# Optimization experiments

Measured on AMD Instinct MI355X. Metric: run time of the kernel, lower is better.

## Reference

```python
import jax, jax.numpy as jnp
import numpy as np

V_NT, V_RULE, E, H = 200, 500, 1024, 1024  # H == E so cat([nt_emb, prod_emb]) == E + H
B, T, L_NL, L_ENV = 32, 128, 512, 512


def setup_inputs() -> dict:
    key = jax.random.key(0)
    ks = jax.random.split(key, 20)
    s = 0.02
    return {
        'init_prod': jax.random.randint(ks[0], (B,), 0, V_RULE),
        'nt_ids': jax.random.randint(ks[1], (T, B), 0, V_NT),
        'h0': jax.random.normal(ks[2], (B, H), jnp.float32),
        'c0': jax.random.normal(ks[3], (B, H), jnp.float32),
        'nl_encoding': jax.random.normal(ks[4], (B, L_NL, H), jnp.float32),
        'env_encoding': jax.random.normal(ks[5], (B, L_ENV, H), jnp.float32),
        'nt_emb': jax.random.normal(ks[6], (V_NT, E), jnp.float32) * s,
        'rule_emb': jax.random.normal(ks[7], (V_RULE, E), jnp.float32) * s,
        'W_ih': jax.random.normal(ks[8], (4 * H, E + H), jnp.float32) * s,
        'W_hh': jax.random.normal(ks[9], (4 * H, H), jnp.float32) * s,
        'b_ih': jnp.zeros((4 * H,), jnp.float32),
        'b_hh': jnp.zeros((4 * H,), jnp.float32),
        'Wz': jax.random.normal(ks[10], (H, 2 * H), jnp.float32) * s,
        'bz': jnp.zeros((H,), jnp.float32),
        'We': jax.random.normal(ks[11], (H, 2 * H), jnp.float32) * s,
        'be': jnp.zeros((H,), jnp.float32),
        'Wc': jax.random.normal(ks[12], (H, 3 * H), jnp.float32) * s,
        'bc': jnp.zeros((H,), jnp.float32),
    }


def _attention(query, context, W, b):
    # query: (B, H), context: (B, L, H)
    scores = jnp.einsum('bh,blh->bl', query, context)          # bmm(output, context^T)
    attn = jax.nn.softmax(scores, axis=-1)                     # softmax over input_len
    mix = jnp.einsum('bl,blh->bh', attn, context)              # bmm(attn, context)
    out = jnp.tanh(jnp.concatenate([mix, query], axis=-1) @ W.T + b)
    return out, attn


def reference(init_prod, nt_ids, h0, c0, nl_encoding, env_encoding,
              nt_emb, rule_emb, W_ih, W_hh, b_ih, b_hh,
              Wz, bz, We, be, Wc, bc):
    last_prod = rule_emb[init_prod]  # (B, E); never updated in the source loop

    def step(carry, nt_t):
        h, c = carry
        x = jnp.concatenate([nt_emb[nt_t], last_prod], axis=-1)  # (B, E+H)
        gates = x @ W_ih.T + b_ih + h @ W_hh.T + b_hh             # (B, 4H)
        i, f, g, o = jnp.split(gates, 4, axis=-1)                 # torch gate order i,f,g,o
        i = jax.nn.sigmoid(i); f = jax.nn.sigmoid(f)
        g = jnp.tanh(g); o = jax.nn.sigmoid(o)
        c_new = f * c + i * g
        h_new = o * jnp.tanh(c_new)
        st = h_new                                                # (B, H)
        zt, _ = _attention(st, nl_encoding, Wz, bz)               # nl cross-attention
        et, _ = _attention(zt, env_encoding, We, be)              # env cross-attention
        ct = jnp.tanh(jnp.concatenate([st, zt, et], axis=-1) @ Wc.T + bc)
        return (h_new, c_new), ct

    _, cts = jax.lax.scan(step, (h0, c0), nt_ids)  # cts: (T, B, H)
    return cts
```

## Files before the change

### kernel.cpp

```cpp
#include <hip/hip_runtime.h>
#include <hip/hip_bf16.h>

typedef _Float16 f16;
typedef __attribute__((ext_vector_type(8))) _Float16 f16x8;
typedef __attribute__((ext_vector_type(4))) float f32x4;
typedef __attribute__((ext_vector_type(4))) unsigned int u32x4;
typedef __attribute__((ext_vector_type(2))) int i32x2;

#define TT 128
#define LSTM_BLOCKS 128

__device__ __forceinline__ float sigmoidf_(float x) { return 1.0f / (1.0f + __expf(-x)); }

__global__ __launch_bounds__(256) void k_f2h(const float* __restrict__ in,
                                             f16* __restrict__ out, long n4) {
  long i = (long)blockIdx.x * 256 + threadIdx.x;
  if (i >= n4) return;
  float4 v = ((const float4*)in)[i];
  out[i*4+0] = (f16)v.x; out[i*4+1] = (f16)v.y;
  out[i*4+2] = (f16)v.z; out[i*4+3] = (f16)v.w;
}

__global__ __launch_bounds__(256) void k_gather_prod(const float* __restrict__ rule_emb,
                                                     const int* __restrict__ init_prod,
                                                     f16* __restrict__ out) {
  int i = blockIdx.x * 256 + threadIdx.x;
  int b = i >> 10, k = i & 1023;
  out[i] = (f16)rule_emb[(long)init_prod[b] * 1024 + k];
}

__global__ __launch_bounds__(256) void k_h0(const float* __restrict__ h0,
                                            f16* __restrict__ st) {
  int i = blockIdx.x * 256 + threadIdx.x;
  int b = i >> 10, k = i & 1023;
  st[(long)(k >> 3) * 256 + b * 8 + (k & 7)] = (f16)h0[i];
}

__global__ __launch_bounds__(256) void k_zero(int* p, int n) {
  for (int i = threadIdx.x; i < n; i += 256) p[i] = 0;
}

__global__ __launch_bounds__(256) void k_transpose(const float* __restrict__ in,
                                                   f16* __restrict__ outT,
                                                   f16* __restrict__ outN) {
  __shared__ float tile[32][33];
  const int b  = blockIdx.z;
  const int l0 = blockIdx.x * 32, h0 = blockIdx.y * 32;
  in   += (long)b * 512 * 1024;
  outT += (long)b * 1024 * 512;
  outN += (long)b * 512 * 1024;
  const int c = threadIdx.x & 31, r = threadIdx.x >> 5;
#pragma unroll
  for (int p = 0; p < 4; ++p) {
    float v = in[(long)(l0 + r + p*8) * 1024 + h0 + c];
    tile[r + p*8][c] = v;
    outN[(long)(l0 + r + p*8) * 1024 + h0 + c] = (f16)v;
  }
  __syncthreads();
#pragma unroll
  for (int p = 0; p < 4; ++p)
    outT[(long)(h0 + r + p*8) * 512 + l0 + c] = (f16)tile[c][r + p*8];
}

__global__ __launch_bounds__(256) void k_gemm(
    const f16* __restrict__ A, long lda, long sA,
    const f16* __restrict__ B, long ldb, long sB,
    float* __restrict__ outF, long ldF, long sF, long sSl,
    f16* __restrict__ outH, long ldH, long sH,
    f16* __restrict__ outH2, long ldH2, long sH2,
    f16* __restrict__ out2, long ld2, long s2,
    const float* __restrict__ bias1, const float* __restrict__ bias2,
    int M, int N, int K, int act, int bmod, int zdiv, int ilv)
{
  __shared__ __align__(16) f16 As[128][40];
  __shared__ __align__(16) f16 Bs[128][40];
  const int tid = threadIdx.x;
  const int w = tid >> 6, lane = tid & 63;
  const int wm = (w & 1) * 64, wn = (w >> 1) * 64;
  const int lr = lane >> 4, lc = lane & 15;
  const long m0 = (long)blockIdx.x * 128;
  const long n0 = (long)blockIdx.y * 128;
  int z = blockIdx.z, batch = z, slice = 0, Ks = K;
  if (zdiv > 1) { batch = z / zdiv; slice = z - batch * zdiv; Ks = K / zdiv; }
  const long kbeg = (long)slice * Ks;
  A += (long)batch * sA;
  B += (long)batch * sB;

  const int rr = tid >> 2, sg = (tid & 3) * 8;
  const int nIt = Ks / 32;

  uint4 pa[2], pb[2];
  {
    long k = kbeg;
    long kb = bmod ? (k & (bmod - 1)) : k;
#pragma unroll
    for (int p = 0; p < 2; ++p) {
      int row = p * 64 + rr;
      uint4 va = {0,0,0,0}, vb = {0,0,0,0};
      if (m0 + row < M) va = *(const uint4*)(A + (m0 + row) * lda + k + sg);
      if (n0 + row < N) vb = *(const uint4*)(B + (n0 + row) * ldb + kb + sg);
      pa[p] = va; pb[p] = vb;
    }
  }

  f32x4 acc[4][4];
#pragma unroll
  for (int i = 0; i < 4; ++i)
#pragma unroll
    for (int j = 0; j < 4; ++j) { f32x4 zz = {0.f,0.f,0.f,0.f}; acc[i][j] = zz; }

  for (int it = 0; it < nIt; ++it) {
#pragma unroll
    for (int p = 0; p < 2; ++p) {
      *(uint4*)&As[p * 64 + rr][sg] = pa[p];
      *(uint4*)&Bs[p * 64 + rr][sg] = pb[p];
    }
    __syncthreads();
    if (it + 1 < nIt) {
      long k = kbeg + (long)(it + 1) * 32;
      long kb = bmod ? (k & (bmod - 1)) : k;
#pragma unroll
      for (int p = 0; p < 2; ++p) {
        int row = p * 64 + rr;
        uint4 va = {0,0,0,0}, vb = {0,0,0,0};
        if (m0 + row < M) va = *(const uint4*)(A + (m0 + row) * lda + k + sg);
        if (n0 + row < N) vb = *(const uint4*)(B + (n0 + row) * ldb + kb + sg);
        pa[p] = va; pb[p] = vb;
      }
    }
    f16x8 af[4], bf[4];
#pragma unroll
    for (int i = 0; i < 4; ++i) af[i] = *(const f16x8*)&As[wm + i*16 + lc][lr * 8];
#pragma unroll
    for (int j = 0; j < 4; ++j) bf[j] = *(const f16x8*)&Bs[wn + j*16 + lc][lr * 8];
#pragma unroll
    for (int i = 0; i < 4; ++i)
#pragma unroll
      for (int j = 0; j < 4; ++j)
        acc[i][j] = __builtin_amdgcn_mfma_f32_16x16x32_f16(af[i], bf[j], acc[i][j], 0, 0, 0);
    __syncthreads();
  }

  if (outF)  outF  += (long)batch * sF + (long)slice * sSl;
  if (outH)  outH  += (long)batch * sH;
  if (outH2) outH2 += (long)batch * sH2;
  if (out2)  out2  += (long)batch * s2;
#pragma unroll
  for (int i = 0; i < 4; ++i)
#pragma unroll
    for (int j = 0; j < 4; ++j)
#pragma unroll
      for (int r = 0; r < 4; ++r) {
        long row = m0 + wm + i * 16 + lr * 4 + r;
        long col = n0 + wn + j * 16 + lc;
        if (row < M && col < N) {
          float v = acc[i][j][r];
          if (bias1) v += bias1[col];
          if (bias2) v += bias2[col];
          if (act)   v = tanhf(v);
          if (outF) {
            long fc = ilv ? ((col & 1023) * 4 + (col >> 10)) : col;
            outF[row * ldF + fc] = v;
          }
          if (outH)  outH[row * ldH + col] = (f16)v;
          if (outH2) outH2[row * ldH2 + col] = (f16)v;
          if (out2) {
            f16 hi = (f16)v;
            out2[row * ld2 + col]        = hi;
            out2[row * ld2 + 1024 + col] = (f16)(v - (float)hi);
          }
        }
      }
}

__global__ __launch_bounds__(256, 1) void k_lstm_all(
    const f16* __restrict__ Whh,
    const float* __restrict__ nt_table,
    const float* __restrict__ prod_gates,
    const int* __restrict__ nt_ids,
    const float* __restrict__ c0,
    f16* __restrict__ st,
    f16* __restrict__ q2,
    f16* __restrict__ X,
    f16* __restrict__ Y1,
    int* __restrict__ flags)
{
  __shared__ __align__(16) f16 whh_s[32][1032];
  __shared__ float partial[2][4][32][34];
  const int tid = threadIdx.x;
  const int w = tid >> 6, lane = tid & 63;
  const int lr = lane >> 4, lc = lane & 15;
  const int bx = blockIdx.x;
  const int j0 = bx * 8;

  for (int i = tid; i < 32 * 128; i += 256) {
    int r = i >> 7, c8 = i & 127;
    int g = r >> 3, jj = r & 7;
    *(uint4*)&whh_s[r][c8 * 8] =
        *(const uint4*)(Whh + ((long)g * 1024 + j0 + jj) * 1024 + c8 * 8);
  }
  const int b_own = tid >> 3, jj_own = tid & 7;
  const int j_own = j0 + jj_own;
  float c_reg = c0[(long)b_own * 1024 + j_own];
  float4 pg4 = *(const float4*)(prod_gates + (long)b_own * 4096 + j_own * 4);
  int nid0 = nt_ids[b_own];
  float4 nt4 = *(const float4*)(nt_table + (long)nid0 * 4096 + j_own * 4);
  __syncthreads();

  f16x8 B0[8], B1[8];
#pragma unroll
  for (int kt = 0; kt < 8; ++kt) {
    int k = w * 256 + kt * 32 + lr * 8;
    B0[kt] = *(const f16x8*)&whh_s[lc][k];
    B1[kt] = *(const f16x8*)&whh_s[16 + lc][k];
  }

  const f16* pA = st + (long)(w * 32 + lr) * 256 + lc * 8;
  const int* fp = flags + w * 128 + lane * 2;

  for (int t = 0; t < TT; ++t) {
    if (t > 0) {
      int done = 0;
      while (true) {
        if (!done) {
          i32x2 ff;
          asm volatile("global_load_dwordx2 %0, %1, off sc0 sc1\n\t"
                       "s_waitcnt vmcnt(0)"
                       : "=&v"(ff) : "v"(fp) : "memory");
          done = (ff.x >= t) & (ff.y >= t);
        }
        if (__all(done)) break;
        __builtin_amdgcn_s_sleep(1);
      }
    }

    u32x4 A0[8], A1[8];
    {
      const f16* pt = pA + (long)t * 32768;
#pragma unroll
      for (int q = 0; q < 4; ++q) {
        asm volatile(
          "global_load_dwordx4 %0, %4, off sc0 sc1\n\t"
          "global_load_dwordx4 %1, %4, off offset:256 sc0 sc1\n\t"
          "global_load_dwordx4 %2, %4, off offset:2048 sc0 sc1\n\t"
          "global_load_dwordx4 %3, %4, off offset:2304 sc0 sc1"
          : "=&v"(A0[2*q]), "=&v"(A1[2*q]), "=&v"(A0[2*q+1]), "=&v"(A1[2*q+1])
          : "v"(pt + (long)q * 2048) : "memory");
      }
      asm volatile("s_waitcnt vmcnt(0)" ::: "memory");
      __builtin_amdgcn_sched_barrier(0);
    }

    float4 nt4n = nt4;
    if (t + 1 < TT) {
      int nidn = nt_ids[(t + 1) * 32 + b_own];
      nt4n = *(const float4*)(nt_table + (long)nidn * 4096 + j_own * 4);
    }

    f32x4 acc[2][2];
#pragma unroll
    for (int i = 0; i < 2; ++i)
#pragma unroll
      for (int j = 0; j < 2; ++j) { f32x4 zz = {0.f,0.f,0.f,0.f}; acc[i][j] = zz; }
#pragma unroll
    for (int kt = 0; kt < 8; ++kt) {
      f16x8 a0v = __builtin_bit_cast(f16x8, A0[kt]);
      f16x8 a1v = __builtin_bit_cast(f16x8, A1[kt]);
      acc[0][0] = __builtin_amdgcn_mfma_f32_16x16x32_f16(a0v, B0[kt], acc[0][0], 0, 0, 0);
      acc[0][1] = __builtin_amdgcn_mfma_f32_16x16x32_f16(a0v, B1[kt], acc[0][1], 0, 0, 0);
      acc[1][0] = __builtin_amdgcn_mfma_f32_16x16x32_f16(a1v, B0[kt], acc[1][0], 0, 0, 0);
      acc[1][1] = __builtin_amdgcn_mfma_f32_16x16x32_f16(a1v, B1[kt], acc[1][1], 0, 0, 0);
    }
    float (*pp)[32][34] = partial[t & 1];
#pragma unroll
    for (int mi = 0; mi < 2; ++mi)
#pragma unroll
      for (int ni = 0; ni < 2; ++ni)
#pragma unroll
        for (int r = 0; r < 4; ++r)
          pp[w][ni * 16 + lc][mi * 16 + lr * 4 + r] = acc[mi][ni][r];
    __syncthreads();

    float g4[4];
#pragma unroll
    for (int g = 0; g < 4; ++g) {
      int rrow = g * 8 + jj_own;
      g4[g] = pp[0][rrow][b_own] + pp[1][rrow][b_own] +
              pp[2][rrow][b_own] + pp[3][rrow][b_own];
    }
    float ii = sigmoidf_(g4[0] + nt4.x + pg4.x);
    float ff = sigmoidf_(g4[1] + nt4.y + pg4.y);
    float gg = tanhf(g4[2] + nt4.z + pg4.z);
    float oo = sigmoidf_(g4[3] + nt4.w + pg4.w);
    c_reg = ff * c_reg + ii * gg;
    float hn = oo * tanhf(c_reg);
    f16 hi = (f16)hn;

    if (t + 1 < TT) {
      union { f16 h; unsigned short u; } cv; cv.h = hi;
      unsigned me = cv.u;
      unsigned d  = me | ((unsigned)__shfl_down((int)me, 1) << 16);
      unsigned d2 = (unsigned)__shfl_down((int)d, 2);
      unsigned e0 = (unsigned)__shfl_down((int)d, 4);
      unsigned e1 = (unsigned)__shfl_down((int)d2, 4);
      if (jj_own == 0) {
        u32x4 pay; pay.x = d; pay.y = d2; pay.z = e0; pay.w = e1;
        f16* pst = st + (long)(t + 1) * 32768 + bx * 256 + b_own * 8;
        asm volatile("global_store_dwordx4 %0, %1, off sc0 sc1"
                     :: "v"(pst), "v"(pay) : "memory");
      }
      asm volatile("s_waitcnt vmcnt(0)" ::: "memory");
      if (lane == 0) {
        int* myf = flags + bx * 4 + w;
        int fv = t + 1;
        asm volatile("global_store_dword %0, %1, off sc0 sc1"
                     :: "v"(myf), "v"(fv) : "memory");
      }
    }

    long row = (long)b_own * 128 + t;
    q2[row * 2048 + j_own]        = hi;
    q2[row * 2048 + 1024 + j_own] = (f16)(hn - (float)hi);
    X[row * 3072 + j_own]         = hi;
    Y1[row * 2048 + 1024 + j_own] = hi;

    nt4 = nt4n;
  }
}

__global__ __launch_bounds__(256) void k_softmax4(const float* __restrict__ p,
                                                  long pstride,
                                                  f16* __restrict__ out) {
  long row = blockIdx.x;
  const float* p0 = p + row * 512;
  out += row * 512;
  const int tid = threadIdx.x, w = tid >> 6, lane = tid & 63;
  float vx = 0.f, vy = 0.f;
#pragma unroll
  for (int s = 0; s < 4; ++s) {
    float2 a = ((const float2*)(p0 + s * pstride))[tid];
    vx += a.x; vy += a.y;
  }
  float m = fmaxf(vx, vy);
#pragma unroll
  for (int off = 32; off; off >>= 1) m = fmaxf(m, __shfl_xor(m, off));
  __shared__ float red[8];
  if (lane == 0) red[w] = m;
  __syncthreads();
  m = fmaxf(fmaxf(red[0], red[1]), fmaxf(red[2], red[3]));
  float e0 = __expf(vx - m), e1 = __expf(vy - m);
  float s2 = e0 + e1;
#pragma unroll
  for (int off = 32; off; off >>= 1) s2 += __shfl_xor(s2, off);
  if (lane == 0) red[4 + w] = s2;
  __syncthreads();
  s2 = red[4] + red[5] + red[6] + red[7];
  float inv = 1.0f / s2;
  out[tid * 2]     = (f16)(e0 * inv);
  out[tid * 2 + 1] = (f16)(e1 * inv);
}

extern "C" void kernel_launch(void* const* d_in, const int* in_sizes, int n_in,
                              void* d_out, int out_size, void* d_ws, size_t ws_size,
                              hipStream_t stream)
{
  const int*   init_prod = (const int*)d_in[0];
  const int*   nt_ids    = (const int*)d_in[1];
  const float* h0   = (const float*)d_in[2];
  const float* c0   = (const float*)d_in[3];
  const float* nl   = (const float*)d_in[4];
  const float* env  = (const float*)d_in[5];
  const float* nt_emb   = (const float*)d_in[6];
  const float* rule_emb = (const float*)d_in[7];
  const float* W_ih = (const float*)d_in[8];
  const float* W_hh = (const float*)d_in[9];
  const float* b_ih = (const float*)d_in[10];
  const float* b_hh = (const float*)d_in[11];
  const float* Wz   = (const float*)d_in[12];
  const float* bz   = (const float*)d_in[13];
  const float* We   = (const float*)d_in[14];
  const float* be   = (const float*)d_in[15];
  const float* Wc   = (const float*)d_in[16];
  const float* bc   = (const float*)d_in[17];
  float* out = (float*)d_out;
  (void)in_sizes; (void)n_in; (void)out_size; (void)ws_size;

  size_t off = 0;
  auto carve = [&](size_t bytes) {
    char* p = (char*)d_ws + off;
    off += (bytes + 255) & ~(size_t)255;
    return (void*)p;
  };
  f16*   Whh_h   = (f16*)carve(4096L * 1024 * 2);
  f16*   Wz_h    = (f16*)carve(1024L * 2048 * 2);
  f16*   We_h    = (f16*)carve(1024L * 2048 * 2);
  f16*   Wc_h    = (f16*)carve(1024L * 3072 * 2);
  f16*   nte_h   = (f16*)carve(200L * 1024 * 2);
  f16*   prod_h  = (f16*)carve(32L * 1024 * 2);
  float* nt_table   = (float*)carve(200L * 4096 * 4);
  float* prod_gates = (float*)carve(32L * 4096 * 4);
  f16*   st_hi   = (f16*)carve(129L * 128 * 32 * 8 * 2);
  f16*   q2      = (f16*)carve(4096L * 2048 * 2);
  f16*   X       = (f16*)carve(4096L * 3072 * 2);
  f16*   Y1      = (f16*)carve(4096L * 2048 * 2);
  f16*   Y2      = (f16*)carve(4096L * 2048 * 2);
  f16*   ctx_h   = (f16*)carve(32L * 512 * 1024 * 2);
  f16*   ctxT    = (f16*)carve(32L * 1024 * 512 * 2);
  float* scoresP = (float*)carve(4L * 32 * 128 * 512 * 4);
  f16*   attn    = (f16*)carve(4096L * 512 * 2);
  int*   bar     = (int*)carve(2048);
  f16*   Wih_h   = (f16*)X;

  auto f2h = [&](const float* src, f16* dst, long n) {
    long n4 = n / 4;
    k_f2h<<<dim3((unsigned)((n4 + 255) / 256)), dim3(256), 0, stream>>>(src, dst, n4);
  };
  f2h(W_ih, Wih_h, 4096L * 2048);
  f2h(W_hh, Whh_h, 4096L * 1024);
  f2h(Wz,   Wz_h,  1024L * 2048);
  f2h(We,   We_h,  1024L * 2048);
  f2h(Wc,   Wc_h,  1024L * 3072);
  f2h(nt_emb, nte_h, 200L * 1024);
  k_gather_prod<<<dim3(128), dim3(256), 0, stream>>>(rule_emb, init_prod, prod_h);
  k_h0<<<dim3(128), dim3(256), 0, stream>>>(h0, st_hi);
  k_zero<<<dim3(1), dim3(256), 0, stream>>>(bar, 512);

  auto gemm = [&](const f16* A, long lda, long sA,
                  const f16* B, long ldb, long sB,
                  float* oF, long ldF, long sF, long sSl,
                  f16* oH, long ldH, long sH,
                  f16* oH2, long ldH2, long sH2,
                  f16* o2, long ld2, long s2,
                  const float* b1, const float* b2,
                  int M, int N, int K, int act, int bmod, int zdiv, int ilv,
                  int batch) {
    dim3 grid((unsigned)((M + 127) / 128), (unsigned)((N + 127) / 128),
              (unsigned)(batch * zdiv));
    k_gemm<<<grid, dim3(256), 0, stream>>>(A, lda, sA, B, ldb, sB,
                                           oF, ldF, sF, sSl, oH, ldH, sH,
                                           oH2, ldH2, sH2, o2, ld2, s2,
                                           b1, b2, M, N, K, act, bmod, zdiv, ilv);
  };
  const long SPL = 32L * 128 * 512;

  gemm(nte_h, 1024, 0, Wih_h, 2048, 0, nt_table, 4096, 0, 0,
       nullptr,0,0, nullptr,0,0, nullptr,0,0, nullptr, nullptr,
       200, 4096, 1024, 0, 0, 1, 1, 1);
  gemm(prod_h, 1024, 0, Wih_h + 1024, 2048, 0, prod_gates, 4096, 0, 0,
       nullptr,0,0, nullptr,0,0, nullptr,0,0, b_ih, b_hh,
       32, 4096, 1024, 0, 0, 1, 1, 1);

  k_lstm_all<<<dim3(LSTM_BLOCKS), dim3(256), 0, stream>>>(
      Whh_h, nt_table, prod_gates, nt_ids, c0, st_hi, q2, X, Y1, bar);

  k_transpose<<<dim3(16, 32, 32), dim3(256), 0, stream>>>(nl, ctxT, ctx_h);
  gemm(q2, 2048, 128L * 2048, ctx_h, 1024, 512L * 1024,
       scoresP, 512, 128L * 512, SPL, nullptr,0,0, nullptr,0,0, nullptr,0,0,
       nullptr, nullptr, 128, 512, 2048, 0, 1024, 4, 0, 32);
  k_softmax4<<<dim3(4096), dim3(256), 0, stream>>>(scoresP, SPL, attn);
  gemm(attn, 512, 128L * 512, ctxT, 512, 1024L * 512,
       nullptr,0,0,0, Y1, 2048, 128L * 2048, nullptr,0,0, nullptr,0,0,
       nullptr, nullptr, 128, 1024, 512, 0, 0, 1, 0, 32);
  gemm(Y1, 2048, 0, Wz_h, 2048, 0,
       nullptr,0,0,0, X + 1024, 3072, 0, Y2 + 1024, 2048, 0, q2, 2048, 0,
       bz, nullptr, 4096, 1024, 2048, 1, 0, 1, 0, 1);

  k_transpose<<<dim3(16, 32, 32), dim3(256), 0, stream>>>(env, ctxT, ctx_h);
  gemm(q2, 2048, 128L * 2048, ctx_h, 1024, 512L * 1024,
       scoresP, 512, 128L * 512, SPL, nullptr,0,0, nullptr,0,0, nullptr,0,0,
       nullptr, nullptr, 128, 512, 2048, 0, 1024, 4, 0, 32);
  k_softmax4<<<dim3(4096), dim3(256), 0, stream>>>(scoresP, SPL, attn);
  gemm(attn, 512, 128L * 512, ctxT, 512, 1024L * 512,
       nullptr,0,0,0, Y2, 2048, 128L * 2048, nullptr,0,0, nullptr,0,0,
       nullptr, nullptr, 128, 1024, 512, 0, 0, 1, 0, 32);
  gemm(Y2, 2048, 0, We_h, 2048, 0,
       nullptr,0,0,0, X + 2048, 3072, 0, nullptr,0,0, nullptr,0,0,
       be, nullptr, 4096, 1024, 2048, 1, 0, 1, 0, 1);

  gemm(X, 3072, 128L * 3072, Wc_h, 3072, 0,
       out, 32L * 1024, 1024, 0, nullptr,0,0, nullptr,0,0, nullptr,0,0,
       bc, nullptr, 128, 1024, 3072, 1, 0, 1, 0, 32);
}
```

Before: 1.147 ms.

## Restructure persistent LSTM into 64 blocks with poisoned-data readiness checks

The recurrent LSTM kernel is repartitioned from 128 blocks of 256 threads into 64 blocks of 512 threads, each owning 16 batch rows and 32 hidden units. W_hh fragments now load directly into registers, and the hidden-state buffer gets a new layout. Cross-block synchronisation uses per-timestep flags, and the hidden-state slots are pre-filled with 0xFFFF so consumers can spin on the data itself until no NaN-pattern values remain. This drops the store-then-flag wait on the producer side. Outputs are written as packed half pairs. The poison-fill and flag-zeroing kernels add pre-pass memory traffic, and the data-polling scheme relies on a freshly computed fp16 value never equalling 0xFFFF.

```diff
diff --git a/kernel.cpp b/kernel.cpp
--- a/kernel.cpp
+++ b/kernel.cpp
@@ -5,12 +5,16 @@
 typedef __attribute__((ext_vector_type(8))) _Float16 f16x8;
 typedef __attribute__((ext_vector_type(4))) float f32x4;
 typedef __attribute__((ext_vector_type(4))) unsigned int u32x4;
-typedef __attribute__((ext_vector_type(2))) int i32x2;
 
 #define TT 128
-#define LSTM_BLOCKS 128
 
 __device__ __forceinline__ float sigmoidf_(float x) { return 1.0f / (1.0f + __expf(-x)); }
+
+__device__ __forceinline__ unsigned pack2h_(float a, float b) {
+  union { f16 h; unsigned short u; } x, y;
+  x.h = (f16)a; y.h = (f16)b;
+  return (unsigned)x.u | ((unsigned)y.u << 16);
+}
 
 __global__ __launch_bounds__(256) void k_f2h(const float* __restrict__ in,
                                              f16* __restrict__ out, long n4) {
@@ -29,15 +33,21 @@
   out[i] = (f16)rule_emb[(long)init_prod[b] * 1024 + k];
 }
 
+__global__ __launch_bounds__(256) void k_poison(unsigned int* __restrict__ p, long n) {
+  long i = (long)blockIdx.x * 256 + threadIdx.x;
+  if (i < n) p[i] = 0xFFFFFFFFu;
+}
+
+__global__ __launch_bounds__(256) void k_zero(int* __restrict__ p, int n) {
+  int i = blockIdx.x * 256 + threadIdx.x;
+  if (i < n) p[i] = 0;
+}
+
 __global__ __launch_bounds__(256) void k_h0(const float* __restrict__ h0,
                                             f16* __restrict__ st) {
   int i = blockIdx.x * 256 + threadIdx.x;
-  int b = i >> 10, k = i & 1023;
-  st[(long)(k >> 3) * 256 + b * 8 + (k & 7)] = (f16)h0[i];
-}
-
-__global__ __launch_bounds__(256) void k_zero(int* p, int n) {
-  for (int i = threadIdx.x; i < n; i += 256) p[i] = 0;
+  int b = i >> 10, j = i & 1023;
+  st[(long)((j >> 5) * 32 + b) * 32 + (j & 31)] = (f16)h0[i];
 }
 
 __global__ __launch_bounds__(256) void k_transpose(const float* __restrict__ in,
@@ -173,7 +183,7 @@
       }
 }
 
-__global__ __launch_bounds__(256, 1) void k_lstm_all(
+__global__ __launch_bounds__(512) void k_lstm_all(
     const f16* __restrict__ Whh,
     const float* __restrict__ nt_table,
     const float* __restrict__ prod_gates,
@@ -185,109 +195,114 @@
     f16* __restrict__ Y1,
     int* __restrict__ flags)
 {
-  __shared__ __align__(16) f16 whh_s[32][1032];
-  __shared__ float partial[2][4][32][34];
+  __shared__ float partial[2][8][128][17];
   const int tid = threadIdx.x;
   const int w = tid >> 6, lane = tid & 63;
   const int lr = lane >> 4, lc = lane & 15;
-  const int bx = blockIdx.x;
-  const int j0 = bx * 8;
-
-  for (int i = tid; i < 32 * 128; i += 256) {
-    int r = i >> 7, c8 = i & 127;
-    int g = r >> 3, jj = r & 7;
-    *(uint4*)&whh_s[r][c8 * 8] =
-        *(const uint4*)(Whh + ((long)g * 1024 + j0 + jj) * 1024 + c8 * 8);
-  }
-  const int b_own = tid >> 3, jj_own = tid & 7;
-  const int j_own = j0 + jj_own;
-  float c_reg = c0[(long)b_own * 1024 + j_own];
-  float4 pg4 = *(const float4*)(prod_gates + (long)b_own * 4096 + j_own * 4);
-  int nid0 = nt_ids[b_own];
+  const int bg = blockIdx.x >> 5;
+  const int cg = blockIdx.x & 31;
+
+  f16x8 Bf[8][4];
+#pragma unroll
+  for (int nt = 0; nt < 8; ++nt) {
+    int n = nt * 16 + lc;
+    const f16* wrow = Whh + (long)((n & 3) * 1024 + cg * 32 + (n >> 2)) * 1024;
+#pragma unroll
+    for (int kt = 0; kt < 4; ++kt)
+      Bf[nt][kt] = *(const f16x8*)(wrow + w * 128 + kt * 32 + lr * 8);
+  }
+
+  const int bl = tid >> 5;
+  const int bglob = bg * 16 + bl;
+  const int c_own = tid & 31;
+  const int j_own = cg * 32 + c_own;
+  float c_reg = c0[(long)bglob * 1024 + j_own];
+  float4 pg4 = *(const float4*)(prod_gates + (long)bglob * 4096 + j_own * 4);
+  int nid0 = nt_ids[bglob];
   float4 nt4 = *(const float4*)(nt_table + (long)nid0 * 4096 + j_own * 4);
-  __syncthreads();
-
-  f16x8 B0[8], B1[8];
-#pragma unroll
-  for (int kt = 0; kt < 8; ++kt) {
-    int k = w * 256 + kt * 32 + lr * 8;
-    B0[kt] = *(const f16x8*)&whh_s[lc][k];
-    B1[kt] = *(const f16x8*)&whh_s[16 + lc][k];
-  }
-
-  const f16* pA = st + (long)(w * 32 + lr) * 256 + lc * 8;
-  const int* fp = flags + w * 128 + lane * 2;
+
+  const f16* pA0 = st + ((long)(w * 4) * 32 + bg * 16 + lc) * 32 + lr * 8;
+  const int* pF = flags + (w * 4 + ((lane >> 3) & 3)) * 16 + bg * 8 + (lane & 7);
 
   for (int t = 0; t < TT; ++t) {
     if (t > 0) {
-      int done = 0;
+      const int* fpt = pF + (long)t * 512;
+      int fdone = (lane >= 32);
       while (true) {
-        if (!done) {
-          i32x2 ff;
-          asm volatile("global_load_dwordx2 %0, %1, off sc0 sc1\n\t"
+        if (!fdone) {
+          int fv;
+          asm volatile("global_load_dword %0, %1, off sc0 sc1\n\t"
                        "s_waitcnt vmcnt(0)"
-                       : "=&v"(ff) : "v"(fp) : "memory");
-          done = (ff.x >= t) & (ff.y >= t);
+                       : "=&v"(fv) : "v"(fpt) : "memory");
+          fdone = (fv != 0);
         }
-        if (__all(done)) break;
+        if (__all(fdone)) break;
         __builtin_amdgcn_s_sleep(1);
       }
     }
 
-    u32x4 A0[8], A1[8];
+    u32x4 Ar[4];
     {
-      const f16* pt = pA + (long)t * 32768;
-#pragma unroll
-      for (int q = 0; q < 4; ++q) {
+      const f16* p0 = pA0 + (long)t * 32768;
+      const f16* p2 = p0 + 2048;
+      while (true) {
         asm volatile(
           "global_load_dwordx4 %0, %4, off sc0 sc1\n\t"
-          "global_load_dwordx4 %1, %4, off offset:256 sc0 sc1\n\t"
-          "global_load_dwordx4 %2, %4, off offset:2048 sc0 sc1\n\t"
-          "global_load_dwordx4 %3, %4, off offset:2304 sc0 sc1"
-          : "=&v"(A0[2*q]), "=&v"(A1[2*q]), "=&v"(A0[2*q+1]), "=&v"(A1[2*q+1])
-          : "v"(pt + (long)q * 2048) : "memory");
-      }
-      asm volatile("s_waitcnt vmcnt(0)" ::: "memory");
+          "global_load_dwordx4 %1, %4, off offset:2048 sc0 sc1\n\t"
+          "global_load_dwordx4 %2, %5, off sc0 sc1\n\t"
+          "global_load_dwordx4 %3, %5, off offset:2048 sc0 sc1\n\t"
+          "s_waitcnt vmcnt(0)"
+          : "=&v"(Ar[0]), "=&v"(Ar[1]), "=&v"(Ar[2]), "=&v"(Ar[3])
+          : "v"(p0), "v"(p2) : "memory");
+        unsigned mA = 0, mB = 0, mC = 0, mD = 0;
+#pragma unroll
+        for (int kt = 0; kt < 4; ++kt) {
+          asm("v_pk_max_u16 %0, %0, %1" : "+v"(mA) : "v"(Ar[kt].x));
+          asm("v_pk_max_u16 %0, %0, %1" : "+v"(mB) : "v"(Ar[kt].y));
+          asm("v_pk_max_u16 %0, %0, %1" : "+v"(mC) : "v"(Ar[kt].z));
+          asm("v_pk_max_u16 %0, %0, %1" : "+v"(mD) : "v"(Ar[kt].w));
+        }
+        asm("v_pk_max_u16 %0, %0, %1" : "+v"(mA) : "v"(mB));
+        asm("v_pk_max_u16 %0, %0, %1" : "+v"(mC) : "v"(mD));
+        asm("v_pk_max_u16 %0, %0, %1" : "+v"(mA) : "v"(mC));
+        int ok = !(((mA & 0xFFFFu) == 0xFFFFu) || ((mA >> 16) == 0xFFFFu));
+        if (__all(ok)) break;
+        __builtin_amdgcn_s_sleep(1);
+      }
       __builtin_amdgcn_sched_barrier(0);
     }
 
     float4 nt4n = nt4;
     if (t + 1 < TT) {
-      int nidn = nt_ids[(t + 1) * 32 + b_own];
+      int nidn = nt_ids[(t + 1) * 32 + bglob];
       nt4n = *(const float4*)(nt_table + (long)nidn * 4096 + j_own * 4);
     }
 
-    f32x4 acc[2][2];
-#pragma unroll
-    for (int i = 0; i < 2; ++i)
-#pragma unroll
-      for (int j = 0; j < 2; ++j) { f32x4 zz = {0.f,0.f,0.f,0.f}; acc[i][j] = zz; }
-#pragma unroll
-    for (int kt = 0; kt < 8; ++kt) {
-      f16x8 a0v = __builtin_bit_cast(f16x8, A0[kt]);
-      f16x8 a1v = __builtin_bit_cast(f16x8, A1[kt]);
-      acc[0][0] = __builtin_amdgcn_mfma_f32_16x16x32_f16(a0v, B0[kt], acc[0][0], 0, 0, 0);
-      acc[0][1] = __builtin_amdgcn_mfma_f32_16x16x32_f16(a0v, B1[kt], acc[0][1], 0, 0, 0);
-      acc[1][0] = __builtin_amdgcn_mfma_f32_16x16x32_f16(a1v, B0[kt], acc[1][0], 0, 0, 0);
-      acc[1][1] = __builtin_amdgcn_mfma_f32_16x16x32_f16(a1v, B1[kt], acc[1][1], 0, 0, 0);
-    }
-    float (*pp)[32][34] = partial[t & 1];
-#pragma unroll
-    for (int mi = 0; mi < 2; ++mi)
-#pragma unroll
-      for (int ni = 0; ni < 2; ++ni)
-#pragma unroll
-        for (int r = 0; r < 4; ++r)
-          pp[w][ni * 16 + lc][mi * 16 + lr * 4 + r] = acc[mi][ni][r];
+    f32x4 acc[8];
+#pragma unroll
+    for (int nt = 0; nt < 8; ++nt) { f32x4 zz = {0.f,0.f,0.f,0.f}; acc[nt] = zz; }
+#pragma unroll
+    for (int kt = 0; kt < 4; ++kt) {
+      f16x8 av = __builtin_bit_cast(f16x8, Ar[kt]);
+#pragma unroll
+      for (int nt = 0; nt < 8; ++nt)
+        acc[nt] = __builtin_amdgcn_mfma_f32_16x16x32_f16(av, Bf[nt][kt], acc[nt], 0, 0, 0);
+    }
+    float (*pp)[128][17] = partial[t & 1];
+#pragma unroll
+    for (int nt = 0; nt < 8; ++nt)
+#pragma unroll
+      for (int r = 0; r < 4; ++r)
+        pp[w][nt * 16 + lc][lr * 4 + r] = acc[nt][r];
     __syncthreads();
 
-    float g4[4];
-#pragma unroll
-    for (int g = 0; g < 4; ++g) {
-      int rrow = g * 8 + jj_own;
-      g4[g] = pp[0][rrow][b_own] + pp[1][rrow][b_own] +
-              pp[2][rrow][b_own] + pp[3][rrow][b_own];
-    }
+    float g4[4] = {0.f, 0.f, 0.f, 0.f};
+#pragma unroll
+    for (int w8 = 0; w8 < 8; ++w8)
+#pragma unroll
+      for (int g = 0; g < 4; ++g)
+        g4[g] += pp[w8][c_own * 4 + g][bl];
+
     float ii = sigmoidf_(g4[0] + nt4.x + pg4.x);
     float ff = sigmoidf_(g4[1] + nt4.y + pg4.y);
     float gg = tanhf(g4[2] + nt4.z + pg4.z);
@@ -295,34 +310,33 @@
     c_reg = ff * c_reg + ii * gg;
     float hn = oo * tanhf(c_reg);
     f16 hi = (f16)hn;
+    float lo_f = hn - (float)hi;
+
+    float hn1 = __shfl_down(hn, 1);
+    float lo1 = __shfl_down(lo_f, 1);
 
     if (t + 1 < TT) {
-      union { f16 h; unsigned short u; } cv; cv.h = hi;
-      unsigned me = cv.u;
-      unsigned d  = me | ((unsigned)__shfl_down((int)me, 1) << 16);
-      unsigned d2 = (unsigned)__shfl_down((int)d, 2);
-      unsigned e0 = (unsigned)__shfl_down((int)d, 4);
-      unsigned e1 = (unsigned)__shfl_down((int)d2, 4);
-      if (jj_own == 0) {
-        u32x4 pay; pay.x = d; pay.y = d2; pay.z = e0; pay.w = e1;
-        f16* pst = st + (long)(t + 1) * 32768 + bx * 256 + b_own * 8;
-        asm volatile("global_store_dwordx4 %0, %1, off sc0 sc1"
+      if (!(tid & 1)) {
+        unsigned pay = pack2h_(hn, hn1);
+        f16* pst = st + ((long)((t + 1) * 32 + cg) * 32 + bglob) * 32 + c_own;
+        asm volatile("global_store_dword %0, %1, off sc0 sc1"
                      :: "v"(pst), "v"(pay) : "memory");
       }
-      asm volatile("s_waitcnt vmcnt(0)" ::: "memory");
       if (lane == 0) {
-        int* myf = flags + bx * 4 + w;
-        int fv = t + 1;
+        int* pf = flags + ((long)(t + 1) * 32 + cg) * 16 + bg * 8 + w;
+        int one = 1;
         asm volatile("global_store_dword %0, %1, off sc0 sc1"
-                     :: "v"(myf), "v"(fv) : "memory");
-      }
-    }
-
-    long row = (long)b_own * 128 + t;
-    q2[row * 2048 + j_own]        = hi;
-    q2[row * 2048 + 1024 + j_own] = (f16)(hn - (float)hi);
-    X[row * 3072 + j_own]         = hi;
-    Y1[row * 2048 + 1024 + j_own] = hi;
+                     :: "v"(pf), "v"(one) : "memory");
+      }
+    }
+
+    if (!(tid & 1)) {
+      long row = (long)bglob * 128 + t;
+      *(unsigned*)&q2[row * 2048 + j_own]        = pack2h_(hn, hn1);
+      *(unsigned*)&q2[row * 2048 + 1024 + j_own] = pack2h_(lo_f, lo1);
+      *(unsigned*)&X[row * 3072 + j_own]         = pack2h_(hn, hn1);
+      *(unsigned*)&Y1[row * 2048 + 1024 + j_own] = pack2h_(hn, hn1);
+    }
 
     nt4 = nt4n;
   }
@@ -399,7 +413,7 @@
   f16*   prod_h  = (f16*)carve(32L * 1024 * 2);
   float* nt_table   = (float*)carve(200L * 4096 * 4);
   float* prod_gates = (float*)carve(32L * 4096 * 4);
-  f16*   st_hi   = (f16*)carve(129L * 128 * 32 * 8 * 2);
+  f16*   st_hi   = (f16*)carve(129L * 32 * 32 * 32 * 2);
   f16*   q2      = (f16*)carve(4096L * 2048 * 2);
   f16*   X       = (f16*)carve(4096L * 3072 * 2);
   f16*   Y1      = (f16*)carve(4096L * 2048 * 2);
@@ -408,7 +422,7 @@
   f16*   ctxT    = (f16*)carve(32L * 1024 * 512 * 2);
   float* scoresP = (float*)carve(4L * 32 * 128 * 512 * 4);
   f16*   attn    = (f16*)carve(4096L * 512 * 2);
-  int*   bar     = (int*)carve(2048);
+  int*   bar     = (int*)carve(129L * 512 * 4);
   f16*   Wih_h   = (f16*)X;
 
   auto f2h = [&](const float* src, f16* dst, long n) {
@@ -422,8 +436,10 @@
   f2h(Wc,   Wc_h,  1024L * 3072);
   f2h(nt_emb, nte_h, 200L * 1024);
   k_gather_prod<<<dim3(128), dim3(256), 0, stream>>>(rule_emb, init_prod, prod_h);
+  k_poison<<<dim3(8192), dim3(256), 0, stream>>>(
+      (unsigned int*)st_hi + 16384, 128L * 16384);
   k_h0<<<dim3(128), dim3(256), 0, stream>>>(h0, st_hi);
-  k_zero<<<dim3(1), dim3(256), 0, stream>>>(bar, 512);
+  k_zero<<<dim3(259), dim3(256), 0, stream>>>(bar, 129 * 512);
 
   auto gemm = [&](const f16* A, long lda, long sA,
                   const f16* B, long ldb, long sB,
@@ -450,7 +466,7 @@
        nullptr,0,0, nullptr,0,0, nullptr,0,0, b_ih, b_hh,
        32, 4096, 1024, 0, 0, 1, 1, 1);
 
-  k_lstm_all<<<dim3(LSTM_BLOCKS), dim3(256), 0, stream>>>(
+  k_lstm_all<<<dim3(64), dim3(512), 0, stream>>>(
       Whh_h, nt_table, prod_gates, nt_ids, c0, st_hi, q2, X, Y1, bar);
 
   k_transpose<<<dim3(16, 32, 32), dim3(256), 0, stream>>>(nl, ctxT, ctx_h);
```

After: 1.234 ms. 7.5% more time.

## Overlap context transposes with LSTM and read fp32 context directly in score GEMM

Applied to the files above, without the earlier changes.

Merges the weight conversion, gather, h0 and flag-zeroing kernels into one grid-stride prep kernel. Moves the nl/env context transposes into 128 extra blocks of the sequential LSTM kernel so they run alongside the recurrence on otherwise idle CUs. The score GEMM now loads the fp32 context and converts it to fp16 inline, which removes the non-transposed fp16 copy. Risks: the LSTM kernel drops its launch_bounds occupancy hint and now shares the GPU with the transpose blocks. Its spin-wait flags also assume all LSTM blocks are co-resident, which the extra blocks could disturb.

```diff
diff --git a/kernel.cpp b/kernel.cpp
--- a/kernel.cpp
+++ b/kernel.cpp
@@ -8,58 +8,48 @@
 typedef __attribute__((ext_vector_type(2))) int i32x2;
 
 #define TT 128
-#define LSTM_BLOCKS 128
 
 __device__ __forceinline__ float sigmoidf_(float x) { return 1.0f / (1.0f + __expf(-x)); }
 
-__global__ __launch_bounds__(256) void k_f2h(const float* __restrict__ in,
-                                             f16* __restrict__ out, long n4) {
-  long i = (long)blockIdx.x * 256 + threadIdx.x;
-  if (i >= n4) return;
-  float4 v = ((const float4*)in)[i];
-  out[i*4+0] = (f16)v.x; out[i*4+1] = (f16)v.y;
-  out[i*4+2] = (f16)v.z; out[i*4+3] = (f16)v.w;
-}
-
-__global__ __launch_bounds__(256) void k_gather_prod(const float* __restrict__ rule_emb,
-                                                     const int* __restrict__ init_prod,
-                                                     f16* __restrict__ out) {
-  int i = blockIdx.x * 256 + threadIdx.x;
-  int b = i >> 10, k = i & 1023;
-  out[i] = (f16)rule_emb[(long)init_prod[b] * 1024 + k];
-}
-
-__global__ __launch_bounds__(256) void k_h0(const float* __restrict__ h0,
-                                            f16* __restrict__ st) {
-  int i = blockIdx.x * 256 + threadIdx.x;
-  int b = i >> 10, k = i & 1023;
-  st[(long)(k >> 3) * 256 + b * 8 + (k & 7)] = (f16)h0[i];
-}
-
-__global__ __launch_bounds__(256) void k_zero(int* p, int n) {
-  for (int i = threadIdx.x; i < n; i += 256) p[i] = 0;
-}
-
-__global__ __launch_bounds__(256) void k_transpose(const float* __restrict__ in,
-                                                   f16* __restrict__ outT,
-                                                   f16* __restrict__ outN) {
-  __shared__ float tile[32][33];
-  const int b  = blockIdx.z;
-  const int l0 = blockIdx.x * 32, h0 = blockIdx.y * 32;
-  in   += (long)b * 512 * 1024;
-  outT += (long)b * 1024 * 512;
-  outN += (long)b * 512 * 1024;
-  const int c = threadIdx.x & 31, r = threadIdx.x >> 5;
-#pragma unroll
-  for (int p = 0; p < 4; ++p) {
-    float v = in[(long)(l0 + r + p*8) * 1024 + h0 + c];
-    tile[r + p*8][c] = v;
-    outN[(long)(l0 + r + p*8) * 1024 + h0 + c] = (f16)v;
-  }
-  __syncthreads();
-#pragma unroll
-  for (int p = 0; p < 4; ++p)
-    outT[(long)(h0 + r + p*8) * 512 + l0 + c] = (f16)tile[c][r + p*8];
+__global__ __launch_bounds__(256) void k_prep(
+    const float* __restrict__ W_ih, const float* __restrict__ W_hh,
+    const float* __restrict__ Wz, const float* __restrict__ We,
+    const float* __restrict__ Wc, const float* __restrict__ nt_emb,
+    const float* __restrict__ rule_emb, const int* __restrict__ init_prod,
+    const float* __restrict__ h0,
+    f16* __restrict__ Wih_h, f16* __restrict__ Whh_h,
+    f16* __restrict__ Wz_h, f16* __restrict__ We_h, f16* __restrict__ Wc_h,
+    f16* __restrict__ nte_h, f16* __restrict__ prod_h,
+    f16* __restrict__ st, int* __restrict__ bar)
+{
+  const long nWih = 2097152, nWhh = 1048576, nWz = 524288, nWe = 524288,
+             nWc = 786432, nNte = 51200, nGat = 32768, nH0 = 32768, nZ = 512;
+  const long T0 = nWih, T1 = T0 + nWhh, T2 = T1 + nWz, T3 = T2 + nWe,
+             T4 = T3 + nWc, T5 = T4 + nNte, T6 = T5 + nGat, T7 = T6 + nH0,
+             T8 = T7 + nZ;
+  const long stride = (long)gridDim.x * 256;
+  for (long i = (long)blockIdx.x * 256 + threadIdx.x; i < T8; i += stride) {
+    if (i < T5) {
+      const float* src; f16* dst; long j;
+      if (i < T0)      { src = W_ih;   dst = Wih_h; j = i; }
+      else if (i < T1) { src = W_hh;   dst = Whh_h; j = i - T0; }
+      else if (i < T2) { src = Wz;     dst = Wz_h;  j = i - T1; }
+      else if (i < T3) { src = We;     dst = We_h;  j = i - T2; }
+      else if (i < T4) { src = Wc;     dst = Wc_h;  j = i - T3; }
+      else             { src = nt_emb; dst = nte_h; j = i - T4; }
+      float4 v = ((const float4*)src)[j];
+      dst[j*4+0] = (f16)v.x; dst[j*4+1] = (f16)v.y;
+      dst[j*4+2] = (f16)v.z; dst[j*4+3] = (f16)v.w;
+    } else if (i < T6) {
+      long j = i - T5; int b = (int)(j >> 10), k = (int)(j & 1023);
+      prod_h[j] = (f16)rule_emb[(long)init_prod[b] * 1024 + k];
+    } else if (i < T7) {
+      long j = i - T6; int b = (int)(j >> 10), k = (int)(j & 1023);
+      st[(long)(k >> 3) * 256 + b * 8 + (k & 7)] = (f16)h0[j];
+    } else {
+      bar[i - T7] = 0;
+    }
+  }
 }
 
 __global__ __launch_bounds__(256) void k_gemm(
@@ -70,7 +60,7 @@
     f16* __restrict__ outH2, long ldH2, long sH2,
     f16* __restrict__ out2, long ld2, long s2,
     const float* __restrict__ bias1, const float* __restrict__ bias2,
-    int M, int N, int K, int act, int bmod, int zdiv, int ilv)
+    int M, int N, int K, int act, int bmod, int zdiv, int ilv, int bf32)
 {
   __shared__ __align__(16) f16 As[128][40];
   __shared__ __align__(16) f16 Bs[128][40];
@@ -84,10 +74,32 @@
   if (zdiv > 1) { batch = z / zdiv; slice = z - batch * zdiv; Ks = K / zdiv; }
   const long kbeg = (long)slice * Ks;
   A += (long)batch * sA;
-  B += (long)batch * sB;
+  const float* B32 = nullptr;
+  if (bf32) B32 = (const float*)B + (long)batch * sB;
+  else      B += (long)batch * sB;
 
   const int rr = tid >> 2, sg = (tid & 3) * 8;
   const int nIt = Ks / 32;
+
+  auto loadB = [&](int row, long kb) -> uint4 {
+    uint4 vb = {0,0,0,0};
+    if (n0 + row < N) {
+      if (bf32) {
+        const float* p = B32 + (n0 + row) * ldb + kb + sg;
+        float4 v0 = *(const float4*)p;
+        float4 v1 = *(const float4*)(p + 4);
+        union { f16 h[8]; uint4 u; } cv;
+        cv.h[0] = (f16)v0.x; cv.h[1] = (f16)v0.y;
+        cv.h[2] = (f16)v0.z; cv.h[3] = (f16)v0.w;
+        cv.h[4] = (f16)v1.x; cv.h[5] = (f16)v1.y;
+        cv.h[6] = (f16)v1.z; cv.h[7] = (f16)v1.w;
+        vb = cv.u;
+      } else {
+        vb = *(const uint4*)(B + (n0 + row) * ldb + kb + sg);
+      }
+    }
+    return vb;
+  };
 
   uint4 pa[2], pb[2];
   {
@@ -96,10 +108,9 @@
 #pragma unroll
     for (int p = 0; p < 2; ++p) {
       int row = p * 64 + rr;
-      uint4 va = {0,0,0,0}, vb = {0,0,0,0};
+      uint4 va = {0,0,0,0};
       if (m0 + row < M) va = *(const uint4*)(A + (m0 + row) * lda + k + sg);
-      if (n0 + row < N) vb = *(const uint4*)(B + (n0 + row) * ldb + kb + sg);
-      pa[p] = va; pb[p] = vb;
+      pa[p] = va; pb[p] = loadB(row, kb);
     }
   }
 
@@ -122,10 +133,9 @@
 #pragma unroll
       for (int p = 0; p < 2; ++p) {
         int row = p * 64 + rr;
-        uint4 va = {0,0,0,0}, vb = {0,0,0,0};
+        uint4 va = {0,0,0,0};
         if (m0 + row < M) va = *(const uint4*)(A + (m0 + row) * lda + k + sg);
-        if (n0 + row < N) vb = *(const uint4*)(B + (n0 + row) * ldb + kb + sg);
-        pa[p] = va; pb[p] = vb;
+        pa[p] = va; pb[p] = loadB(row, kb);
       }
     }
     f16x8 af[4], bf[4];
@@ -173,7 +183,7 @@
       }
 }
 
-__global__ __launch_bounds__(256, 1) void k_lstm_all(
+__global__ __launch_bounds__(256) void k_lstm_all(
     const f16* __restrict__ Whh,
     const float* __restrict__ nt_table,
     const float* __restrict__ prod_gates,
@@ -183,14 +193,44 @@
     f16* __restrict__ q2,
     f16* __restrict__ X,
     f16* __restrict__ Y1,
-    int* __restrict__ flags)
+    int* __restrict__ flags,
+    const float* __restrict__ nl,
+    const float* __restrict__ env,
+    f16* __restrict__ ctxT_nl, f16* __restrict__ ctxT_env)
 {
   __shared__ __align__(16) f16 whh_s[32][1032];
   __shared__ float partial[2][4][32][34];
+  __shared__ float tile[32][33];
   const int tid = threadIdx.x;
+  const int bx = blockIdx.x;
+
+  if (bx >= 128) {
+    const int me = bx - 128;
+    const int c = tid & 31, r = tid >> 5;
+#pragma unroll
+    for (int pass = 0; pass < 2; ++pass) {
+      const float* in = pass ? env : nl;
+      f16* oT = pass ? ctxT_env : ctxT_nl;
+      for (int idx = me; idx < 16384; idx += 128) {
+        int b = idx >> 9, rr2 = idx & 511;
+        int l0 = (rr2 & 15) * 32, h0v = (rr2 >> 4) * 32;
+        const float* inb = in + (long)b * 512 * 1024;
+        f16* oTb = oT + (long)b * 1024 * 512;
+#pragma unroll
+        for (int p = 0; p < 4; ++p)
+          tile[r + p*8][c] = inb[(long)(l0 + r + p*8) * 1024 + h0v + c];
+        __syncthreads();
+#pragma unroll
+        for (int p = 0; p < 4; ++p)
+          oTb[(long)(h0v + r + p*8) * 512 + l0 + c] = (f16)tile[c][r + p*8];
+        __syncthreads();
+      }
+    }
+    return;
+  }
+
   const int w = tid >> 6, lane = tid & 63;
   const int lr = lane >> 4, lc = lane & 15;
-  const int bx = blockIdx.x;
   const int j0 = bx * 8;
 
   for (int i = tid; i < 32 * 128; i += 256) {
@@ -298,8 +338,8 @@
 
     if (t + 1 < TT) {
       union { f16 h; unsigned short u; } cv; cv.h = hi;
-      unsigned me = cv.u;
-      unsigned d  = me | ((unsigned)__shfl_down((int)me, 1) << 16);
+      unsigned me2 = cv.u;
+      unsigned d  = me2 | ((unsigned)__shfl_down((int)me2, 1) << 16);
       unsigned d2 = (unsigned)__shfl_down((int)d, 2);
       unsigned e0 = (unsigned)__shfl_down((int)d, 4);
       unsigned e1 = (unsigned)__shfl_down((int)d2, 4);
@@ -404,26 +444,16 @@
   f16*   X       = (f16*)carve(4096L * 3072 * 2);
   f16*   Y1      = (f16*)carve(4096L * 2048 * 2);
   f16*   Y2      = (f16*)carve(4096L * 2048 * 2);
-  f16*   ctx_h   = (f16*)carve(32L * 512 * 1024 * 2);
-  f16*   ctxT    = (f16*)carve(32L * 1024 * 512 * 2);
+  f16*   ctxT_nl  = (f16*)carve(32L * 1024 * 512 * 2);
+  f16*   ctxT_env = (f16*)carve(32L * 1024 * 512 * 2);
   float* scoresP = (float*)carve(4L * 32 * 128 * 512 * 4);
   f16*   attn    = (f16*)carve(4096L * 512 * 2);
   int*   bar     = (int*)carve(2048);
   f16*   Wih_h   = (f16*)X;
 
-  auto f2h = [&](const float* src, f16* dst, long n) {
-    long n4 = n / 4;
-    k_f2h<<<dim3((unsigned)((n4 + 255) / 256)), dim3(256), 0, stream>>>(src, dst, n4);
-  };
-  f2h(W_ih, Wih_h, 4096L * 2048);
-  f2h(W_hh, Whh_h, 4096L * 1024);
-  f2h(Wz,   Wz_h,  1024L * 2048);
-  f2h(We,   We_h,  1024L * 2048);
-  f2h(Wc,   Wc_h,  1024L * 3072);
-  f2h(nt_emb, nte_h, 200L * 1024);
-  k_gather_prod<<<dim3(128), dim3(256), 0, stream>>>(rule_emb, init_prod, prod_h);
-  k_h0<<<dim3(128), dim3(256), 0, stream>>>(h0, st_hi);
-  k_zero<<<dim3(1), dim3(256), 0, stream>>>(bar, 512);
+  k_prep<<<dim3(8192), dim3(256), 0, stream>>>(
+      W_ih, W_hh, Wz, We, Wc, nt_emb, rule_emb, init_prod, h0,
+      Wih_h, Whh_h, Wz_h, We_h, Wc_h, nte_h, prod_h, st_hi, bar);
 
   auto gemm = [&](const f16* A, long lda, long sA,
                   const f16* B, long ldb, long sB,
@@ -433,51 +463,51 @@
                   f16* o2, long ld2, long s2,
                   const float* b1, const float* b2,
                   int M, int N, int K, int act, int bmod, int zdiv, int ilv,
-                  int batch) {
+                  int bf32, int batch) {
     dim3 grid((unsigned)((M + 127) / 128), (unsigned)((N + 127) / 128),
               (unsigned)(batch * zdiv));
     k_gemm<<<grid, dim3(256), 0, stream>>>(A, lda, sA, B, ldb, sB,
                                            oF, ldF, sF, sSl, oH, ldH, sH,
                                            oH2, ldH2, sH2, o2, ld2, s2,
-                                           b1, b2, M, N, K, act, bmod, zdiv, ilv);
+                                           b1, b2, M, N, K, act, bmod, zdiv,
+                                           ilv, bf32);
   };
   const long SPL = 32L * 128 * 512;
 
   gemm(nte_h, 1024, 0, Wih_h, 2048, 0, nt_table, 4096, 0, 0,
        nullptr,0,0, nullptr,0,0, nullptr,0,0, nullptr, nullptr,
-       200, 4096, 1024, 0, 0, 1, 1, 1);
+       200, 4096, 1024, 0, 0, 1, 1, 0, 1);
   gemm(prod_h, 1024, 0, Wih_h + 1024, 2048, 0, prod_gates, 4096, 0, 0,
        nullptr,0,0, nullptr,0,0, nullptr,0,0, b_ih, b_hh,
-       32, 4096, 1024, 0, 0, 1, 1, 1);
-
-  k_lstm_all<<<dim3(LSTM_BLOCKS), dim3(256), 0, stream>>>(
-      Whh_h, nt_table, prod_gates, nt_ids, c0, st_hi, q2, X, Y1, bar);
-
-  k_transpose<<<dim3(16, 32, 32), dim3(256), 0, stream>>>(nl, ctxT, ctx_h);
-  gemm(q2, 2048, 128L * 2048, ctx_h, 1024, 512L * 1024,
+       32, 4096, 1024, 0, 0, 1, 1, 0, 1);
+
+  k_lstm_all<<<dim3(256), dim3(256), 0, stream>>>(
+      Whh_h, nt_table, prod_gates, nt_ids, c0, st_hi, q2, X, Y1, bar,
+      nl, env, ctxT_nl, ctxT_env);
+
+  gemm(q2, 2048, 128L * 2048, (const f16*)nl, 1024, 512L * 1024,
        scoresP, 512, 128L * 512, SPL, nullptr,0,0, nullptr,0,0, nullptr,0,0,
-       nullptr, nullptr, 128, 512, 2048, 0, 1024, 4, 0, 32);
+       nullptr, nullptr, 128, 512, 2048, 0, 1024, 4, 0, 1, 32);
   k_softmax4<<<dim3(4096), dim3(256), 0, stream>>>(scoresP, SPL, attn);
-  gemm(attn, 512, 128L * 512, ctxT, 512, 1024L * 512,
+  gemm(attn, 512, 128L * 512, ctxT_nl, 512, 1024L * 512,
        nullptr,0,0,0, Y1, 2048, 128L * 2048, nullptr,0,0, nullptr,0,0,
-       nullptr, nullptr, 128, 1024, 512, 0, 0, 1, 0, 32);
+       nullptr, nullptr, 128, 1024, 512, 0, 0, 1, 0, 0, 32);
   gemm(Y1, 2048, 0, Wz_h, 2048, 0,
        nullptr,0,0,0, X + 1024, 3072, 0, Y2 + 1024, 2048, 0, q2, 2048, 0,
-       bz, nullptr, 4096, 1024, 2048, 1, 0, 1, 0, 1);
-
-  k_transpose<<<dim3(16, 32, 32), dim3(256), 0, stream>>>(env, ctxT, ctx_h);
-  gemm(q2, 2048, 128L * 2048, ctx_h, 1024, 512L * 1024,
+       bz, nullptr, 4096, 1024, 2048, 1, 0, 1, 0, 0, 1);
+
+  gemm(q2, 2048, 128L * 2048, (const f16*)env, 1024, 512L * 1024,
        scoresP, 512, 128L * 512, SPL, nullptr,0,0, nullptr,0,0, nullptr,0,0,
-       nullptr, nullptr, 128, 512, 2048, 0, 1024, 4, 0, 32);
+       nullptr, nullptr, 128, 512, 2048, 0, 1024, 4, 0, 1, 32);
   k_softmax4<<<dim3(4096), dim3(256), 0, stream>>>(scoresP, SPL, attn);
-  gemm(attn, 512, 128L * 512, ctxT, 512, 1024L * 512,
+  gemm(attn, 512, 128L * 512, ctxT_env, 512, 1024L * 512,
        nullptr,0,0,0, Y2, 2048, 128L * 2048, nullptr,0,0, nullptr,0,0,
-       nullptr, nullptr, 128, 1024, 512, 0, 0, 1, 0, 32);
+       nullptr, nullptr, 128, 1024, 512, 0, 0, 1, 0, 0, 32);
   gemm(Y2, 2048, 0, We_h, 2048, 0,
        nullptr,0,0,0, X + 2048, 3072, 0, nullptr,0,0, nullptr,0,0,
-       be, nullptr, 4096, 1024, 2048, 1, 0, 1, 0, 1);
+       be, nullptr, 4096, 1024, 2048, 1, 0, 1, 0, 0, 1);
 
   gemm(X, 3072, 128L * 3072, Wc_h, 3072, 0,
        out, 32L * 1024, 1024, 0, nullptr,0,0, nullptr,0,0, nullptr,0,0,
-       bc, nullptr, 128, 1024, 3072, 1, 0, 1, 0, 32);
+       bc, nullptr, 128, 1024, 3072, 1, 0, 1, 0, 0, 32);
 }
```

Measured after the change: 1.270 ms. +10.7%, slower.
